# Kernel tuning notes

Measured on AMD Instinct MI355X. Metric: run time of the kernel, lower is better.

Reference implementation:

```python
import jax, jax.numpy as jnp
import numpy as np

BLOCK = 16
N1, N2, RANK = 64, 64, 64
# E2M1 (NVFP4) representable magnitudes
_FP4_GRID = jnp.array([0.0, 0.5, 1.0, 1.5, 2.0, 3.0, 4.0, 6.0], dtype=jnp.float32)
_FP4_MIDS = (_FP4_GRID[1:] + _FP4_GRID[:-1]) / 2.0


def quantize_to_nvfp4(x, block_size=BLOCK):
    """Per-block (last dim, block_size=16) NVFP4 fake-quant: amax scale to 6.0, round to E2M1 grid, dequant."""
    shape = x.shape
    xb = x.reshape(shape[:-1] + (shape[-1] // block_size, block_size))
    amax = jnp.max(jnp.abs(xb), axis=-1, keepdims=True)
    scale = jnp.maximum(amax / 6.0, 1e-8)
    y = xb / scale
    idx = jnp.searchsorted(_FP4_MIDS, jnp.abs(y), side='right')  # nearest grid index
    q = _FP4_GRID[idx] * jnp.sign(y)
    return (q * scale).reshape(shape)


def setup_inputs() -> dict:
    key = jax.random.key(0)
    ks = jax.random.split(key, 6)
    B, S, n, m, r = 4, 2048, 4096, 4096, RANK
    return {
        'x': jax.random.normal(ks[0], (B, S, n), dtype=jnp.float32),
        'smooth_scale': jax.random.uniform(ks[1], (n,), dtype=jnp.float32, minval=0.2, maxval=2.0),
        'a_q': jax.random.normal(ks[2], (m, r), dtype=jnp.float32) * 0.05,
        'b_q': jax.random.normal(ks[3], (N1, r), dtype=jnp.float32) * 0.1,
        'c_q_t': jax.random.normal(ks[4], (r, N2), dtype=jnp.float32) * 0.1,
        'bias': jax.random.normal(ks[5], (m,), dtype=jnp.float32),
    }


def reference(x, smooth_scale, a_q, b_q, c_q_t, bias):
    # smooth + activation quant
    x_q = quantize_to_nvfp4(x * smooth_scale, BLOCK)
    # reshape (..., n) -> (..., n1, n2)
    x_3d = x_q.reshape(x.shape[:-1] + (N1, N2))
    # contract C: F.linear(x_3d, c_q_t) -> (..., n1, r)
    h1 = jnp.einsum('bsij,rj->bsir', x_3d, c_q_t)
    # contract B: (h1 * B).sum over n1 -> (..., r)
    h2 = jnp.einsum('bsir,ir->bsr', h1, b_q)
    # contract A: h2 @ A.T + bias -> (..., m)
    out = jnp.einsum('bsr,mr->bsm', h2, a_q) + bias
    return out
```

## Files before the change

### kernel.cpp

```cpp
#include <hip/hip_runtime.h>

typedef float f32x4 __attribute__((ext_vector_type(4)));
typedef short s16x8 __attribute__((ext_vector_type(8)));
typedef short s16x4 __attribute__((ext_vector_type(4)));
typedef unsigned short u16;

#define N_COLS 4096
#define RANK 64

__device__ __forceinline__ unsigned f_asuint(float f) { union { float f; unsigned u; } v; v.f = f; return v.u; }
__device__ __forceinline__ float f_asfloat(unsigned u) { union { unsigned u; float f; } v; v.u = u; return v.f; }
__device__ __forceinline__ short f2bf(float f) {
  unsigned u = f_asuint(f);
  return (short)((u + 0x7fffu + ((u >> 16) & 1u)) >> 16);
}

__global__ __launch_bounds__(256) void k_prep(const float* __restrict__ b_q,
                                              const float* __restrict__ c_q_t,
                                              const float* __restrict__ a_q,
                                              u16* __restrict__ W,
                                              u16* __restrict__ a_bf) {
  int idx = blockIdx.x * 256 + threadIdx.x;
  if (idx < RANK * N_COLS) {
    int r = idx >> 12;
    int n = idx & 4095;
    W[idx] = (u16)f2bf(b_q[(n >> 6) * RANK + r] * c_q_t[(r << 6) + (n & 63)]);
  } else {
    int j = idx - RANK * N_COLS;
    a_bf[j] = (u16)f2bf(a_q[j]);
  }
}

__global__ __launch_bounds__(512, 4) void k_qgemm1(const float* __restrict__ x,
                                                   const float* __restrict__ smooth,
                                                   const u16* __restrict__ W,
                                                   u16* __restrict__ h2b) {
  const int t0 = blockIdx.x * 16;
  const int wave = threadIdx.x >> 6;
  const int lane = threadIdx.x & 63;
  const int quad = lane >> 4;
  const int tl = lane & 15;
  const int K0 = wave * 512 + quad * 8;

  const float* xp = x + (size_t)(t0 + tl) * N_COLS + K0;
  const float* sp = smooth + K0;
  const u16* wp0 = W + (size_t)tl * N_COLS + K0;
  const u16* wp1 = wp0 + 16 * N_COLS;
  const u16* wp2 = wp0 + 32 * N_COLS;
  const u16* wp3 = wp0 + 48 * N_COLS;

  f32x4 acc0 = {0.f, 0.f, 0.f, 0.f};
  f32x4 acc1 = {0.f, 0.f, 0.f, 0.f};
  f32x4 acc2 = {0.f, 0.f, 0.f, 0.f};
  f32x4 acc3 = {0.f, 0.f, 0.f, 0.f};

  for (int s = 0; s < 16; ++s) {
    const int o = s * 32;
    f32x4 xa = __builtin_nontemporal_load(reinterpret_cast<const f32x4*>(xp + o));
    f32x4 xb = __builtin_nontemporal_load(reinterpret_cast<const f32x4*>(xp + o + 4));
    f32x4 sa = *reinterpret_cast<const f32x4*>(sp + o);
    f32x4 sb = *reinterpret_cast<const f32x4*>(sp + o + 4);
    float xs[8];
    xs[0] = xa.x * sa.x; xs[1] = xa.y * sa.y; xs[2] = xa.z * sa.z; xs[3] = xa.w * sa.w;
    xs[4] = xb.x * sb.x; xs[5] = xb.y * sb.y; xs[6] = xb.z * sb.z; xs[7] = xb.w * sb.w;

    float amax = fabsf(xs[0]);
#pragma unroll
    for (int j = 1; j < 8; ++j) amax = fmaxf(amax, fabsf(xs[j]));
    amax = fmaxf(amax, __shfl_xor(amax, 16));
    float scale = fmaxf(amax * (1.0f / 6.0f), 1e-8f);

    const float th0 = 0.25f * scale, th1 = 0.75f * scale, th2 = 1.25f * scale,
                th3 = 1.75f * scale, th4 = 2.5f * scale, th5 = 3.5f * scale,
                th6 = 5.0f * scale;
    s16x8 af;
#pragma unroll
    for (int j = 0; j < 8; ++j) {
      float ax = fabsf(xs[j]);
      float q = (ax >= th0) ? 0.5f : 0.0f;
      q = (ax >= th1) ? 1.0f : q;
      q = (ax >= th2) ? 1.5f : q;
      q = (ax >= th3) ? 2.0f : q;
      q = (ax >= th4) ? 3.0f : q;
      q = (ax >= th5) ? 4.0f : q;
      q = (ax >= th6) ? 6.0f : q;
      float xq = q * scale;
      xq = f_asfloat(f_asuint(xq) | (f_asuint(xs[j]) & 0x80000000u));
      af[j] = f2bf(xq);
    }

    s16x8 b0 = *reinterpret_cast<const s16x8*>(wp0 + o);
    s16x8 b1 = *reinterpret_cast<const s16x8*>(wp1 + o);
    s16x8 b2 = *reinterpret_cast<const s16x8*>(wp2 + o);
    s16x8 b3 = *reinterpret_cast<const s16x8*>(wp3 + o);

    acc0 = __builtin_amdgcn_mfma_f32_16x16x32_bf16(af, b0, acc0, 0, 0, 0);
    acc1 = __builtin_amdgcn_mfma_f32_16x16x32_bf16(af, b1, acc1, 0, 0, 0);
    acc2 = __builtin_amdgcn_mfma_f32_16x16x32_bf16(af, b2, acc2, 0, 0, 0);
    acc3 = __builtin_amdgcn_mfma_f32_16x16x32_bf16(af, b3, acc3, 0, 0, 0);
  }

  __shared__ float red[8 * 16 * 64];
  float* rw = red + wave * 1024 + (quad * 4) * 64 + tl;
#pragma unroll
  for (int reg = 0; reg < 4; ++reg) {
    rw[reg * 64 + 0]  = acc0[reg];
    rw[reg * 64 + 16] = acc1[reg];
    rw[reg * 64 + 32] = acc2[reg];
    rw[reg * 64 + 48] = acc3[reg];
  }
  __syncthreads();
  if (threadIdx.x < 256) {
    const f32x4* r4 = reinterpret_cast<const f32x4*>(red);
    f32x4 v = r4[threadIdx.x];
#pragma unroll
    for (int p = 1; p < 8; ++p) {
      f32x4 u = r4[p * 256 + threadIdx.x];
      v.x += u.x; v.y += u.y; v.z += u.z; v.w += u.w;
    }
    int t = threadIdx.x >> 4;
    int rr = (threadIdx.x & 15) * 4;
    s16x4 o4;
    o4.x = f2bf(v.x); o4.y = f2bf(v.y); o4.z = f2bf(v.z); o4.w = f2bf(v.w);
    *reinterpret_cast<s16x4*>(h2b + (size_t)(t0 + t) * RANK + rr) = o4;
  }
}

__global__ __launch_bounds__(256, 4) void k_gemm2(const u16* __restrict__ h2b,
                                                  const u16* __restrict__ a_bf,
                                                  const float* __restrict__ bias,
                                                  float* __restrict__ out) {
  const int t0 = blockIdx.y * 32;
  const int m0 = blockIdx.x * 256;
  const int wave = threadIdx.x >> 6;
  const int lane = threadIdx.x & 63;
  const int quad = lane >> 4;
  const int tl = lane & 15;

  const u16* hp0 = h2b + (size_t)(t0 + tl) * RANK + quad * 8;
  const u16* hp1 = hp0 + 16 * RANK;
  const u16* ap = a_bf + (size_t)(m0 + wave * 64 + tl) * RANK + quad * 8;

  f32x4 acc[2][4] = {};

#pragma unroll
  for (int o = 0; o < 64; o += 32) {
    s16x8 a0 = *reinterpret_cast<const s16x8*>(hp0 + o);
    s16x8 a1 = *reinterpret_cast<const s16x8*>(hp1 + o);
#pragma unroll
    for (int mg = 0; mg < 4; ++mg) {
      s16x8 bfr = *reinterpret_cast<const s16x8*>(ap + (size_t)mg * 16 * RANK + o);
      acc[0][mg] = __builtin_amdgcn_mfma_f32_16x16x32_bf16(a0, bfr, acc[0][mg], 0, 0, 0);
      acc[1][mg] = __builtin_amdgcn_mfma_f32_16x16x32_bf16(a1, bfr, acc[1][mg], 0, 0, 0);
    }
  }

  __shared__ float tile[16 * 260];
#pragma unroll
  for (int tg = 0; tg < 2; ++tg) {
    if (tg) __syncthreads();
#pragma unroll
    for (int mg = 0; mg < 4; ++mg)
#pragma unroll
      for (int reg = 0; reg < 4; ++reg)
        tile[(quad * 4 + reg) * 260 + wave * 64 + mg * 16 + tl] = acc[tg][mg][reg];
    __syncthreads();
#pragma unroll
    for (int i = 0; i < 4; ++i) {
      int idx = threadIdx.x + i * 256;
      int row = idx >> 6;
      int c4 = (idx & 63) << 2;
      f32x4 v = *reinterpret_cast<const f32x4*>(tile + row * 260 + c4);
      f32x4 b = *reinterpret_cast<const f32x4*>(bias + m0 + c4);
      f32x4 ov;
      ov.x = v.x + b.x; ov.y = v.y + b.y; ov.z = v.z + b.z; ov.w = v.w + b.w;
      __builtin_nontemporal_store(ov,
        reinterpret_cast<f32x4*>(out + (size_t)(t0 + tg * 16 + row) * N_COLS + m0 + c4));
    }
  }
}

extern "C" void kernel_launch(void* const* d_in, const int* in_sizes, int n_in,
                              void* d_out, int out_size, void* d_ws, size_t ws_size,
                              hipStream_t stream) {
  const float* x      = (const float*)d_in[0];
  const float* smooth = (const float*)d_in[1];
  const float* a_q    = (const float*)d_in[2];
  const float* b_q    = (const float*)d_in[3];
  const float* c_q_t  = (const float*)d_in[4];
  const float* bias   = (const float*)d_in[5];
  float* out = (float*)d_out;

  const int T = in_sizes[0] / N_COLS;

  u16* W    = (u16*)d_ws;
  u16* a_bf = (u16*)((char*)d_ws + 524288);
  u16* h2b  = (u16*)((char*)d_ws + 1048576);

  k_prep<<<2048, 256, 0, stream>>>(b_q, c_q_t, a_q, W, a_bf);
  k_qgemm1<<<T / 16, 512, 0, stream>>>(x, smooth, W, h2b);
  dim3 g2(N_COLS / 256, T / 32);
  k_gemm2<<<g2, 256, 0, stream>>>(h2b, a_bf, bias, out);
}
```

Measured before the change: 278.4 us.

## Fuse quantized GEMM1 and rank-64 GEMM2 into one kernel via LDS

Merges the quantize+first contraction kernel with the output GEMM so each 16-token block keeps its rank-64 intermediate in shared memory and writes the bias-added output directly. This removes the h2 round trip through global memory and one kernel launch. The output stage uses a swizzled LDS staging tile per wave. The prep kernel is also vectorized to process 8 elements per thread. In exchange, the output write phase now runs inside the same blocks that stream x, so per-block work grows and the load and store phases serialize within a block.

```diff
diff --git a/kernel.cpp b/kernel.cpp
--- a/kernel.cpp
+++ b/kernel.cpp
@@ -20,96 +20,114 @@
                                               const float* __restrict__ a_q,
                                               u16* __restrict__ W,
                                               u16* __restrict__ a_bf) {
-  int idx = blockIdx.x * 256 + threadIdx.x;
-  if (idx < RANK * N_COLS) {
-    int r = idx >> 12;
-    int n = idx & 4095;
-    W[idx] = (u16)f2bf(b_q[(n >> 6) * RANK + r] * c_q_t[(r << 6) + (n & 63)]);
+  int j = blockIdx.x * 256 + threadIdx.x;
+  if (j < 32768) {
+    int r = j >> 9;
+    int n0 = (j << 3) & 4095;
+    float b = b_q[(n0 >> 6) * RANK + r];
+    const f32x4* cp = reinterpret_cast<const f32x4*>(c_q_t + (r << 6) + (n0 & 63));
+    f32x4 c0 = cp[0], c1 = cp[1];
+    s16x8 w;
+    w[0] = f2bf(b * c0.x); w[1] = f2bf(b * c0.y); w[2] = f2bf(b * c0.z); w[3] = f2bf(b * c0.w);
+    w[4] = f2bf(b * c1.x); w[5] = f2bf(b * c1.y); w[6] = f2bf(b * c1.z); w[7] = f2bf(b * c1.w);
+    *reinterpret_cast<s16x8*>(W + ((size_t)j << 3)) = w;
   } else {
-    int j = idx - RANK * N_COLS;
-    a_bf[j] = (u16)f2bf(a_q[j]);
-  }
-}
-
-__global__ __launch_bounds__(512, 4) void k_qgemm1(const float* __restrict__ x,
-                                                   const float* __restrict__ smooth,
-                                                   const u16* __restrict__ W,
-                                                   u16* __restrict__ h2b) {
+    int j2 = j - 32768;
+    const f32x4* ap = reinterpret_cast<const f32x4*>(a_q + ((size_t)j2 << 3));
+    f32x4 a0 = ap[0], a1 = ap[1];
+    s16x8 v;
+    v[0] = f2bf(a0.x); v[1] = f2bf(a0.y); v[2] = f2bf(a0.z); v[3] = f2bf(a0.w);
+    v[4] = f2bf(a1.x); v[5] = f2bf(a1.y); v[6] = f2bf(a1.z); v[7] = f2bf(a1.w);
+    *reinterpret_cast<s16x8*>(a_bf + ((size_t)j2 << 3)) = v;
+  }
+}
+
+__global__ __launch_bounds__(512, 4) void k_fused(const float* __restrict__ x,
+                                                  const float* __restrict__ smooth,
+                                                  const u16* __restrict__ W,
+                                                  const u16* __restrict__ a_bf,
+                                                  const float* __restrict__ bias,
+                                                  float* __restrict__ out) {
   const int t0 = blockIdx.x * 16;
   const int wave = threadIdx.x >> 6;
   const int lane = threadIdx.x & 63;
   const int quad = lane >> 4;
   const int tl = lane & 15;
-  const int K0 = wave * 512 + quad * 8;
-
-  const float* xp = x + (size_t)(t0 + tl) * N_COLS + K0;
-  const float* sp = smooth + K0;
-  const u16* wp0 = W + (size_t)tl * N_COLS + K0;
-  const u16* wp1 = wp0 + 16 * N_COLS;
-  const u16* wp2 = wp0 + 32 * N_COLS;
-  const u16* wp3 = wp0 + 48 * N_COLS;
-
-  f32x4 acc0 = {0.f, 0.f, 0.f, 0.f};
-  f32x4 acc1 = {0.f, 0.f, 0.f, 0.f};
-  f32x4 acc2 = {0.f, 0.f, 0.f, 0.f};
-  f32x4 acc3 = {0.f, 0.f, 0.f, 0.f};
-
-  for (int s = 0; s < 16; ++s) {
-    const int o = s * 32;
-    f32x4 xa = __builtin_nontemporal_load(reinterpret_cast<const f32x4*>(xp + o));
-    f32x4 xb = __builtin_nontemporal_load(reinterpret_cast<const f32x4*>(xp + o + 4));
-    f32x4 sa = *reinterpret_cast<const f32x4*>(sp + o);
-    f32x4 sb = *reinterpret_cast<const f32x4*>(sp + o + 4);
-    float xs[8];
-    xs[0] = xa.x * sa.x; xs[1] = xa.y * sa.y; xs[2] = xa.z * sa.z; xs[3] = xa.w * sa.w;
-    xs[4] = xb.x * sb.x; xs[5] = xb.y * sb.y; xs[6] = xb.z * sb.z; xs[7] = xb.w * sb.w;
-
-    float amax = fabsf(xs[0]);
-#pragma unroll
-    for (int j = 1; j < 8; ++j) amax = fmaxf(amax, fabsf(xs[j]));
-    amax = fmaxf(amax, __shfl_xor(amax, 16));
-    float scale = fmaxf(amax * (1.0f / 6.0f), 1e-8f);
-
-    const float th0 = 0.25f * scale, th1 = 0.75f * scale, th2 = 1.25f * scale,
-                th3 = 1.75f * scale, th4 = 2.5f * scale, th5 = 3.5f * scale,
-                th6 = 5.0f * scale;
-    s16x8 af;
-#pragma unroll
-    for (int j = 0; j < 8; ++j) {
-      float ax = fabsf(xs[j]);
-      float q = (ax >= th0) ? 0.5f : 0.0f;
-      q = (ax >= th1) ? 1.0f : q;
-      q = (ax >= th2) ? 1.5f : q;
-      q = (ax >= th3) ? 2.0f : q;
-      q = (ax >= th4) ? 3.0f : q;
-      q = (ax >= th5) ? 4.0f : q;
-      q = (ax >= th6) ? 6.0f : q;
-      float xq = q * scale;
-      xq = f_asfloat(f_asuint(xq) | (f_asuint(xs[j]) & 0x80000000u));
-      af[j] = f2bf(xq);
-    }
-
-    s16x8 b0 = *reinterpret_cast<const s16x8*>(wp0 + o);
-    s16x8 b1 = *reinterpret_cast<const s16x8*>(wp1 + o);
-    s16x8 b2 = *reinterpret_cast<const s16x8*>(wp2 + o);
-    s16x8 b3 = *reinterpret_cast<const s16x8*>(wp3 + o);
-
-    acc0 = __builtin_amdgcn_mfma_f32_16x16x32_bf16(af, b0, acc0, 0, 0, 0);
-    acc1 = __builtin_amdgcn_mfma_f32_16x16x32_bf16(af, b1, acc1, 0, 0, 0);
-    acc2 = __builtin_amdgcn_mfma_f32_16x16x32_bf16(af, b2, acc2, 0, 0, 0);
-    acc3 = __builtin_amdgcn_mfma_f32_16x16x32_bf16(af, b3, acc3, 0, 0, 0);
-  }
-
-  __shared__ float red[8 * 16 * 64];
-  float* rw = red + wave * 1024 + (quad * 4) * 64 + tl;
-#pragma unroll
-  for (int reg = 0; reg < 4; ++reg) {
-    rw[reg * 64 + 0]  = acc0[reg];
-    rw[reg * 64 + 16] = acc1[reg];
-    rw[reg * 64 + 32] = acc2[reg];
-    rw[reg * 64 + 48] = acc3[reg];
+
+  __shared__ float red[8 * 1088];
+  __shared__ u16 h2l[16 * 72];
+
+  {
+    const int K0 = wave * 512 + quad * 8;
+    const float* xp = x + (size_t)(t0 + tl) * N_COLS + K0;
+    const float* sp = smooth + K0;
+    const u16* wp0 = W + (size_t)tl * N_COLS + K0;
+    const u16* wp1 = wp0 + 16 * N_COLS;
+    const u16* wp2 = wp0 + 32 * N_COLS;
+    const u16* wp3 = wp0 + 48 * N_COLS;
+
+    f32x4 acc0 = {0.f, 0.f, 0.f, 0.f};
+    f32x4 acc1 = {0.f, 0.f, 0.f, 0.f};
+    f32x4 acc2 = {0.f, 0.f, 0.f, 0.f};
+    f32x4 acc3 = {0.f, 0.f, 0.f, 0.f};
+
+    for (int s = 0; s < 16; ++s) {
+      const int o = s * 32;
+      f32x4 xa = __builtin_nontemporal_load(reinterpret_cast<const f32x4*>(xp + o));
+      f32x4 xb = __builtin_nontemporal_load(reinterpret_cast<const f32x4*>(xp + o + 4));
+      f32x4 sa = *reinterpret_cast<const f32x4*>(sp + o);
+      f32x4 sb = *reinterpret_cast<const f32x4*>(sp + o + 4);
+      float xs[8];
+      xs[0] = xa.x * sa.x; xs[1] = xa.y * sa.y; xs[2] = xa.z * sa.z; xs[3] = xa.w * sa.w;
+      xs[4] = xb.x * sb.x; xs[5] = xb.y * sb.y; xs[6] = xb.z * sb.z; xs[7] = xb.w * sb.w;
+
+      float amax = fabsf(xs[0]);
+#pragma unroll
+      for (int j = 1; j < 8; ++j) amax = fmaxf(amax, fabsf(xs[j]));
+      amax = fmaxf(amax, __shfl_xor(amax, 16));
+      float scale = fmaxf(amax * (1.0f / 6.0f), 1e-8f);
+
+      const float th0 = 0.25f * scale, th1 = 0.75f * scale, th2 = 1.25f * scale,
+                  th3 = 1.75f * scale, th4 = 2.5f * scale, th5 = 3.5f * scale,
+                  th6 = 5.0f * scale;
+      s16x8 af;
+#pragma unroll
+      for (int j = 0; j < 8; ++j) {
+        float ax = fabsf(xs[j]);
+        float q = (ax >= th0) ? 0.5f : 0.0f;
+        q = (ax >= th1) ? 1.0f : q;
+        q = (ax >= th2) ? 1.5f : q;
+        q = (ax >= th3) ? 2.0f : q;
+        q = (ax >= th4) ? 3.0f : q;
+        q = (ax >= th5) ? 4.0f : q;
+        q = (ax >= th6) ? 6.0f : q;
+        float xq = q * scale;
+        xq = f_asfloat(f_asuint(xq) | (f_asuint(xs[j]) & 0x80000000u));
+        af[j] = f2bf(xq);
+      }
+
+      s16x8 b0 = *reinterpret_cast<const s16x8*>(wp0 + o);
+      s16x8 b1 = *reinterpret_cast<const s16x8*>(wp1 + o);
+      s16x8 b2 = *reinterpret_cast<const s16x8*>(wp2 + o);
+      s16x8 b3 = *reinterpret_cast<const s16x8*>(wp3 + o);
+
+      acc0 = __builtin_amdgcn_mfma_f32_16x16x32_bf16(af, b0, acc0, 0, 0, 0);
+      acc1 = __builtin_amdgcn_mfma_f32_16x16x32_bf16(af, b1, acc1, 0, 0, 0);
+      acc2 = __builtin_amdgcn_mfma_f32_16x16x32_bf16(af, b2, acc2, 0, 0, 0);
+      acc3 = __builtin_amdgcn_mfma_f32_16x16x32_bf16(af, b3, acc3, 0, 0, 0);
+    }
+
+    float* rw = red + wave * 1024 + (quad * 4) * 64 + tl;
+#pragma unroll
+    for (int reg = 0; reg < 4; ++reg) {
+      rw[reg * 64 + 0]  = acc0[reg];
+      rw[reg * 64 + 16] = acc1[reg];
+      rw[reg * 64 + 32] = acc2[reg];
+      rw[reg * 64 + 48] = acc3[reg];
+    }
   }
   __syncthreads();
+
   if (threadIdx.x < 256) {
     const f32x4* r4 = reinterpret_cast<const f32x4*>(red);
     f32x4 v = r4[threadIdx.x];
@@ -121,61 +139,52 @@
     int t = threadIdx.x >> 4;
     int rr = (threadIdx.x & 15) * 4;
     s16x4 o4;
-    o4.x = f2bf(v.x); o4.y = f2bf(v.y); o4.z = f2bf(v.z); o4.w = f2bf(v.w);
-    *reinterpret_cast<s16x4*>(h2b + (size_t)(t0 + t) * RANK + rr) = o4;
-  }
-}
-
-__global__ __launch_bounds__(256, 4) void k_gemm2(const u16* __restrict__ h2b,
-                                                  const u16* __restrict__ a_bf,
-                                                  const float* __restrict__ bias,
-                                                  float* __restrict__ out) {
-  const int t0 = blockIdx.y * 32;
-  const int m0 = blockIdx.x * 256;
-  const int wave = threadIdx.x >> 6;
-  const int lane = threadIdx.x & 63;
-  const int quad = lane >> 4;
-  const int tl = lane & 15;
-
-  const u16* hp0 = h2b + (size_t)(t0 + tl) * RANK + quad * 8;
-  const u16* hp1 = hp0 + 16 * RANK;
-  const u16* ap = a_bf + (size_t)(m0 + wave * 64 + tl) * RANK + quad * 8;
-
-  f32x4 acc[2][4] = {};
-
-#pragma unroll
-  for (int o = 0; o < 64; o += 32) {
-    s16x8 a0 = *reinterpret_cast<const s16x8*>(hp0 + o);
-    s16x8 a1 = *reinterpret_cast<const s16x8*>(hp1 + o);
-#pragma unroll
-    for (int mg = 0; mg < 4; ++mg) {
-      s16x8 bfr = *reinterpret_cast<const s16x8*>(ap + (size_t)mg * 16 * RANK + o);
-      acc[0][mg] = __builtin_amdgcn_mfma_f32_16x16x32_bf16(a0, bfr, acc[0][mg], 0, 0, 0);
-      acc[1][mg] = __builtin_amdgcn_mfma_f32_16x16x32_bf16(a1, bfr, acc[1][mg], 0, 0, 0);
-    }
-  }
-
-  __shared__ float tile[16 * 260];
-#pragma unroll
-  for (int tg = 0; tg < 2; ++tg) {
-    if (tg) __syncthreads();
-#pragma unroll
-    for (int mg = 0; mg < 4; ++mg)
-#pragma unroll
-      for (int reg = 0; reg < 4; ++reg)
-        tile[(quad * 4 + reg) * 260 + wave * 64 + mg * 16 + tl] = acc[tg][mg][reg];
-    __syncthreads();
+    o4[0] = f2bf(v.x); o4[1] = f2bf(v.y); o4[2] = f2bf(v.z); o4[3] = f2bf(v.w);
+    *reinterpret_cast<s16x4*>(h2l + t * 72 + rr) = o4;
+  }
+  __syncthreads();
+
+  s16x8 h0 = *reinterpret_cast<const s16x8*>(h2l + tl * 72 + quad * 8);
+  s16x8 h1 = *reinterpret_cast<const s16x8*>(h2l + tl * 72 + quad * 8 + 32);
+
+  float* wt = red + wave * 1088;
+  const int mstrip = wave * 512;
+  const int r_out = lane >> 2;
+  const int sl = lane & 3;
+
+  for (int mg = 0; mg < 8; ++mg) {
+    const int mbase = mstrip + mg * 64;
+    const u16* ap = a_bf + (size_t)(mbase + tl) * RANK + quad * 8;
+
+    f32x4 acc[4] = {{0.f,0.f,0.f,0.f},{0.f,0.f,0.f,0.f},{0.f,0.f,0.f,0.f},{0.f,0.f,0.f,0.f}};
+#pragma unroll
+    for (int nt = 0; nt < 4; ++nt) {
+      const u16* ap2 = ap + (size_t)nt * 16 * RANK;
+      s16x8 bb0 = *reinterpret_cast<const s16x8*>(ap2);
+      s16x8 bb1 = *reinterpret_cast<const s16x8*>(ap2 + 32);
+      acc[nt] = __builtin_amdgcn_mfma_f32_16x16x32_bf16(h0, bb0, acc[nt], 0, 0, 0);
+      acc[nt] = __builtin_amdgcn_mfma_f32_16x16x32_bf16(h1, bb1, acc[nt], 0, 0, 0);
+    }
+
+#pragma unroll
+    for (int nt = 0; nt < 4; ++nt)
+#pragma unroll
+      for (int reg = 0; reg < 4; ++reg) {
+        int tok = quad * 4 + reg;
+        wt[tok * 68 + ((nt * 16 + tl) ^ ((tok & 3) << 4))] = acc[nt][reg];
+      }
+
+    const f32x4* bp = reinterpret_cast<const f32x4*>(bias + mbase);
+    float* op = out + (size_t)(t0 + r_out) * N_COLS + mbase;
 #pragma unroll
     for (int i = 0; i < 4; ++i) {
-      int idx = threadIdx.x + i * 256;
-      int row = idx >> 6;
-      int c4 = (idx & 63) << 2;
-      f32x4 v = *reinterpret_cast<const f32x4*>(tile + row * 260 + c4);
-      f32x4 b = *reinterpret_cast<const f32x4*>(bias + m0 + c4);
+      int c4 = sl + i * 4;
+      f32x4 v = *reinterpret_cast<const f32x4*>(
+          wt + r_out * 68 + ((c4 * 4) ^ ((r_out & 3) << 4)));
+      f32x4 b = bp[c4];
       f32x4 ov;
       ov.x = v.x + b.x; ov.y = v.y + b.y; ov.z = v.z + b.z; ov.w = v.w + b.w;
-      __builtin_nontemporal_store(ov,
-        reinterpret_cast<f32x4*>(out + (size_t)(t0 + tg * 16 + row) * N_COLS + m0 + c4));
+      __builtin_nontemporal_store(ov, reinterpret_cast<f32x4*>(op + c4 * 4));
     }
   }
 }
@@ -195,10 +204,7 @@
 
   u16* W    = (u16*)d_ws;
   u16* a_bf = (u16*)((char*)d_ws + 524288);
-  u16* h2b  = (u16*)((char*)d_ws + 1048576);
-
-  k_prep<<<2048, 256, 0, stream>>>(b_q, c_q_t, a_q, W, a_bf);
-  k_qgemm1<<<T / 16, 512, 0, stream>>>(x, smooth, W, h2b);
-  dim3 g2(N_COLS / 256, T / 32);
-  k_gemm2<<<g2, 256, 0, stream>>>(h2b, a_bf, bias, out);
-}
+
+  k_prep<<<256, 256, 0, stream>>>(b_q, c_q_t, a_q, W, a_bf);
+  k_fused<<<T / 16, 512, 0, stream>>>(x, smooth, W, a_bf, bias, out);
+}
```

Result: slower. 294.4 us (+5.8%).

## Split K across blocks in first GEMM with register prefetch and fused partial reduction

Applied to the files above, without the earlier changes.

The x·W contraction is split into four K-chunks handled by separate 256-thread blocks. Each block writes fp32 partial h2 results, and gemm2 sums the four partials and converts them to bf16 in shared memory before its MFMA loop. The main loop now software-prefetches x, smooth and W registers several steps ahead instead of loading inside each iteration, and the prep kernel is vectorized to eight elements per thread. The aim is more parallelism and better latency hiding on the memory-bound read of x. The cost is extra global traffic for the fp32 partials, a redundant partial reduction in every gemm2 block, and dropping the nontemporal hint on x.

```diff
diff --git a/kernel.cpp b/kernel.cpp
--- a/kernel.cpp
+++ b/kernel.cpp
@@ -20,28 +20,43 @@
                                               const float* __restrict__ a_q,
                                               u16* __restrict__ W,
                                               u16* __restrict__ a_bf) {
-  int idx = blockIdx.x * 256 + threadIdx.x;
-  if (idx < RANK * N_COLS) {
-    int r = idx >> 12;
-    int n = idx & 4095;
-    W[idx] = (u16)f2bf(b_q[(n >> 6) * RANK + r] * c_q_t[(r << 6) + (n & 63)]);
+  int j = blockIdx.x * 256 + threadIdx.x;
+  if (j < 32768) {
+    int r = j >> 9;
+    int n0 = (j << 3) & 4095;
+    float b = b_q[(n0 >> 6) * RANK + r];
+    const f32x4* cp = reinterpret_cast<const f32x4*>(c_q_t + (r << 6) + (n0 & 63));
+    f32x4 c0 = cp[0], c1 = cp[1];
+    s16x8 w;
+    w[0] = f2bf(b * c0.x); w[1] = f2bf(b * c0.y); w[2] = f2bf(b * c0.z); w[3] = f2bf(b * c0.w);
+    w[4] = f2bf(b * c1.x); w[5] = f2bf(b * c1.y); w[6] = f2bf(b * c1.z); w[7] = f2bf(b * c1.w);
+    *reinterpret_cast<s16x8*>(W + ((size_t)j << 3)) = w;
   } else {
-    int j = idx - RANK * N_COLS;
-    a_bf[j] = (u16)f2bf(a_q[j]);
-  }
-}
-
-__global__ __launch_bounds__(512, 4) void k_qgemm1(const float* __restrict__ x,
-                                                   const float* __restrict__ smooth,
-                                                   const u16* __restrict__ W,
-                                                   u16* __restrict__ h2b) {
+    int j2 = j - 32768;
+    const f32x4* ap = reinterpret_cast<const f32x4*>(a_q + ((size_t)j2 << 3));
+    f32x4 a0 = ap[0], a1 = ap[1];
+    s16x8 v;
+    v[0] = f2bf(a0.x); v[1] = f2bf(a0.y); v[2] = f2bf(a0.z); v[3] = f2bf(a0.w);
+    v[4] = f2bf(a1.x); v[5] = f2bf(a1.y); v[6] = f2bf(a1.z); v[7] = f2bf(a1.w);
+    *reinterpret_cast<s16x8*>(a_bf + ((size_t)j2 << 3)) = v;
+  }
+}
+
+__global__ __launch_bounds__(256, 4) void k_h2(const float* __restrict__ x,
+                                               const float* __restrict__ smooth,
+                                               const u16* __restrict__ W,
+                                               float* __restrict__ h2p,
+                                               int T) {
   const int t0 = blockIdx.x * 16;
+  const int kb = blockIdx.y;
   const int wave = threadIdx.x >> 6;
   const int lane = threadIdx.x & 63;
   const int quad = lane >> 4;
   const int tl = lane & 15;
-  const int K0 = wave * 512 + quad * 8;
-
+
+  __shared__ float red[4 * 1024];
+
+  const int K0 = kb * 1024 + wave * 256 + quad * 8;
   const float* xp = x + (size_t)(t0 + tl) * N_COLS + K0;
   const float* sp = smooth + K0;
   const u16* wp0 = W + (size_t)tl * N_COLS + K0;
@@ -54,12 +69,44 @@
   f32x4 acc2 = {0.f, 0.f, 0.f, 0.f};
   f32x4 acc3 = {0.f, 0.f, 0.f, 0.f};
 
-  for (int s = 0; s < 16; ++s) {
-    const int o = s * 32;
-    f32x4 xa = __builtin_nontemporal_load(reinterpret_cast<const f32x4*>(xp + o));
-    f32x4 xb = __builtin_nontemporal_load(reinterpret_cast<const f32x4*>(xp + o + 4));
-    f32x4 sa = *reinterpret_cast<const f32x4*>(sp + o);
-    f32x4 sb = *reinterpret_cast<const f32x4*>(sp + o + 4);
+  f32x4 pxa[4], pxb[4];
+  f32x4 psa[2], psb[2];
+  s16x8 pw[2][4];
+#pragma unroll
+  for (int s = 0; s < 4; ++s) {
+    pxa[s] = *reinterpret_cast<const f32x4*>(xp + s * 32);
+    pxb[s] = *reinterpret_cast<const f32x4*>(xp + s * 32 + 4);
+  }
+#pragma unroll
+  for (int s = 0; s < 2; ++s) {
+    psa[s] = *reinterpret_cast<const f32x4*>(sp + s * 32);
+    psb[s] = *reinterpret_cast<const f32x4*>(sp + s * 32 + 4);
+    pw[s][0] = *reinterpret_cast<const s16x8*>(wp0 + s * 32);
+    pw[s][1] = *reinterpret_cast<const s16x8*>(wp1 + s * 32);
+    pw[s][2] = *reinterpret_cast<const s16x8*>(wp2 + s * 32);
+    pw[s][3] = *reinterpret_cast<const s16x8*>(wp3 + s * 32);
+  }
+
+#pragma unroll
+  for (int s = 0; s < 8; ++s) {
+    f32x4 xa = pxa[s & 3], xb = pxb[s & 3];
+    f32x4 sa = psa[s & 1], sb = psb[s & 1];
+    s16x8 b0 = pw[s & 1][0], b1 = pw[s & 1][1], b2 = pw[s & 1][2], b3 = pw[s & 1][3];
+
+    if (s + 4 < 8) {
+      pxa[s & 3] = *reinterpret_cast<const f32x4*>(xp + (s + 4) * 32);
+      pxb[s & 3] = *reinterpret_cast<const f32x4*>(xp + (s + 4) * 32 + 4);
+    }
+    if (s + 2 < 8) {
+      const int o2 = (s + 2) * 32;
+      psa[s & 1] = *reinterpret_cast<const f32x4*>(sp + o2);
+      psb[s & 1] = *reinterpret_cast<const f32x4*>(sp + o2 + 4);
+      pw[s & 1][0] = *reinterpret_cast<const s16x8*>(wp0 + o2);
+      pw[s & 1][1] = *reinterpret_cast<const s16x8*>(wp1 + o2);
+      pw[s & 1][2] = *reinterpret_cast<const s16x8*>(wp2 + o2);
+      pw[s & 1][3] = *reinterpret_cast<const s16x8*>(wp3 + o2);
+    }
+
     float xs[8];
     xs[0] = xa.x * sa.x; xs[1] = xa.y * sa.y; xs[2] = xa.z * sa.z; xs[3] = xa.w * sa.w;
     xs[4] = xb.x * sb.x; xs[5] = xb.y * sb.y; xs[6] = xb.z * sb.z; xs[7] = xb.w * sb.w;
@@ -89,18 +136,12 @@
       af[j] = f2bf(xq);
     }
 
-    s16x8 b0 = *reinterpret_cast<const s16x8*>(wp0 + o);
-    s16x8 b1 = *reinterpret_cast<const s16x8*>(wp1 + o);
-    s16x8 b2 = *reinterpret_cast<const s16x8*>(wp2 + o);
-    s16x8 b3 = *reinterpret_cast<const s16x8*>(wp3 + o);
-
     acc0 = __builtin_amdgcn_mfma_f32_16x16x32_bf16(af, b0, acc0, 0, 0, 0);
     acc1 = __builtin_amdgcn_mfma_f32_16x16x32_bf16(af, b1, acc1, 0, 0, 0);
     acc2 = __builtin_amdgcn_mfma_f32_16x16x32_bf16(af, b2, acc2, 0, 0, 0);
     acc3 = __builtin_amdgcn_mfma_f32_16x16x32_bf16(af, b3, acc3, 0, 0, 0);
   }
 
-  __shared__ float red[8 * 16 * 64];
   float* rw = red + wave * 1024 + (quad * 4) * 64 + tl;
 #pragma unroll
   for (int reg = 0; reg < 4; ++reg) {
@@ -110,26 +151,25 @@
     rw[reg * 64 + 48] = acc3[reg];
   }
   __syncthreads();
-  if (threadIdx.x < 256) {
+  {
     const f32x4* r4 = reinterpret_cast<const f32x4*>(red);
     f32x4 v = r4[threadIdx.x];
 #pragma unroll
-    for (int p = 1; p < 8; ++p) {
+    for (int p = 1; p < 4; ++p) {
       f32x4 u = r4[p * 256 + threadIdx.x];
       v.x += u.x; v.y += u.y; v.z += u.z; v.w += u.w;
     }
     int t = threadIdx.x >> 4;
     int rr = (threadIdx.x & 15) * 4;
-    s16x4 o4;
-    o4.x = f2bf(v.x); o4.y = f2bf(v.y); o4.z = f2bf(v.z); o4.w = f2bf(v.w);
-    *reinterpret_cast<s16x4*>(h2b + (size_t)(t0 + t) * RANK + rr) = o4;
-  }
-}
-
-__global__ __launch_bounds__(256, 4) void k_gemm2(const u16* __restrict__ h2b,
+    *reinterpret_cast<f32x4*>(h2p + ((size_t)kb * T + t0 + t) * RANK + rr) = v;
+  }
+}
+
+__global__ __launch_bounds__(256, 4) void k_gemm2(const float* __restrict__ h2p,
                                                   const u16* __restrict__ a_bf,
                                                   const float* __restrict__ bias,
-                                                  float* __restrict__ out) {
+                                                  float* __restrict__ out,
+                                                  int T) {
   const int t0 = blockIdx.y * 32;
   const int m0 = blockIdx.x * 256;
   const int wave = threadIdx.x >> 6;
@@ -137,8 +177,32 @@
   const int quad = lane >> 4;
   const int tl = lane & 15;
 
-  const u16* hp0 = h2b + (size_t)(t0 + tl) * RANK + quad * 8;
-  const u16* hp1 = hp0 + 16 * RANK;
+  __shared__ u16 h2l[32 * 72];
+  __shared__ float tile[16 * 260];
+
+  {
+    int t = threadIdx.x >> 3;
+    int r0 = (threadIdx.x & 7) * 8;
+    const float* p = h2p + (size_t)(t0 + t) * RANK + r0;
+    f32x4 v0 = *reinterpret_cast<const f32x4*>(p);
+    f32x4 v1 = *reinterpret_cast<const f32x4*>(p + 4);
+#pragma unroll
+    for (int kb = 1; kb < 4; ++kb) {
+      const float* q = p + (size_t)kb * T * RANK;
+      f32x4 u0 = *reinterpret_cast<const f32x4*>(q);
+      f32x4 u1 = *reinterpret_cast<const f32x4*>(q + 4);
+      v0.x += u0.x; v0.y += u0.y; v0.z += u0.z; v0.w += u0.w;
+      v1.x += u1.x; v1.y += u1.y; v1.z += u1.z; v1.w += u1.w;
+    }
+    s16x8 h;
+    h[0] = f2bf(v0.x); h[1] = f2bf(v0.y); h[2] = f2bf(v0.z); h[3] = f2bf(v0.w);
+    h[4] = f2bf(v1.x); h[5] = f2bf(v1.y); h[6] = f2bf(v1.z); h[7] = f2bf(v1.w);
+    *reinterpret_cast<s16x8*>(h2l + t * 72 + r0) = h;
+  }
+  __syncthreads();
+
+  const u16* hp0 = h2l + tl * 72 + quad * 8;
+  const u16* hp1 = hp0 + 16 * 72;
   const u16* ap = a_bf + (size_t)(m0 + wave * 64 + tl) * RANK + quad * 8;
 
   f32x4 acc[2][4] = {};
@@ -155,7 +219,6 @@
     }
   }
 
-  __shared__ float tile[16 * 260];
 #pragma unroll
   for (int tg = 0; tg < 2; ++tg) {
     if (tg) __syncthreads();
@@ -193,12 +256,13 @@
 
   const int T = in_sizes[0] / N_COLS;
 
-  u16* W    = (u16*)d_ws;
-  u16* a_bf = (u16*)((char*)d_ws + 524288);
-  u16* h2b  = (u16*)((char*)d_ws + 1048576);
-
-  k_prep<<<2048, 256, 0, stream>>>(b_q, c_q_t, a_q, W, a_bf);
-  k_qgemm1<<<T / 16, 512, 0, stream>>>(x, smooth, W, h2b);
+  u16* W     = (u16*)d_ws;
+  u16* a_bf  = (u16*)((char*)d_ws + 524288);
+  float* h2p = (float*)((char*)d_ws + 1048576);
+
+  k_prep<<<256, 256, 0, stream>>>(b_q, c_q_t, a_q, W, a_bf);
+  dim3 gh(T / 16, 4);
+  k_h2<<<gh, 256, 0, stream>>>(x, smooth, W, h2p, T);
   dim3 g2(N_COLS / 256, T / 32);
-  k_gemm2<<<g2, 256, 0, stream>>>(h2b, a_bf, bias, out);
-}
+  k_gemm2<<<g2, 256, 0, stream>>>(h2p, a_bf, bias, out, T);
+}
```

Result: no change. 275.3 us (-1.1%).
